# Kernel tuning notes

Measured on AMD Instinct MI355X. Metric: run time of the kernel, lower is better.

Reference implementation:

```python
import jax, jax.numpy as jnp
import numpy as np

NEG_INF = -1e30
EPS = 1e-5


def _layernorm(x, g, b):
    m = jnp.mean(x, axis=-1, keepdims=True)
    v = jnp.var(x, axis=-1, keepdims=True)
    return (x - m) * jax.lax.rsqrt(v + EPS) * g + b


def _mlp(x, w1, b1, w2, b2):
    h = jax.nn.gelu(x @ w1.T + b1, approximate=False)
    return h @ w2.T + b2


def _sparse_attn(q, k, v, scale, window):
    # q: [N,H,Q,hd], k/v: [N,H,K,hd]
    scores = jnp.einsum('nhqd,nhkd->nhqk', q, k) * scale
    scores = jnp.clip(scores, -10000.0, 10000.0)
    Q, K = scores.shape[-2], scores.shape[-1]
    i = jnp.arange(Q)[:, None]
    j = jnp.arange(K)[None, :]
    # row i < K: sliding window of radius `window`; row i >= K: fully unmasked
    allowed = (i >= K) | ((j >= i - window) & (j <= i + window))
    scores = jnp.where(allowed, scores, NEG_INF)
    w = jax.nn.softmax(scores, axis=-1)
    w = jnp.nan_to_num(w, nan=0.0, posinf=10000.0, neginf=-10000.0)
    out = jnp.einsum('nhqk,nhkd->nhqd', w, v)
    return jnp.nan_to_num(out, nan=0.0, posinf=10000.0, neginf=-10000.0)


B, T, L, D = 8, 96, 128, 256
H = 2
HD = D // H
FACTOR = 10
WINDOW = 5
DFF = 4 * D


def setup_inputs() -> dict:
    key = jax.random.key(0)
    ks = jax.random.split(key, 16)
    s = 0.02
    inp = {
        'x': jax.random.normal(ks[0], (B, T, L, D), jnp.float32),
        'router': jax.random.normal(ks[1], (L, FACTOR, D), jnp.float32),
        'Wr': jax.random.normal(ks[2], (D, D), jnp.float32) * s,
        'br': jnp.zeros((D,), jnp.float32),
        'Wk': jax.random.normal(ks[3], (D, D), jnp.float32) * s,
        'bk': jnp.zeros((D,), jnp.float32),
        'Wv': jax.random.normal(ks[4], (D, D), jnp.float32) * s,
        'bv': jnp.zeros((D,), jnp.float32),
        'Wq': jax.random.normal(ks[5], (D, D), jnp.float32) * s,
        'bq': jnp.zeros((D,), jnp.float32),
        'g1': jnp.ones((D,), jnp.float32), 'beta1': jnp.zeros((D,), jnp.float32),
        'g2': jnp.ones((D,), jnp.float32), 'beta2': jnp.zeros((D,), jnp.float32),
        'g3': jnp.ones((D,), jnp.float32), 'beta3': jnp.zeros((D,), jnp.float32),
        'm1_w1': jax.random.normal(ks[6], (DFF, D), jnp.float32) * s,
        'm1_b1': jnp.zeros((DFF,), jnp.float32),
        'm1_w2': jax.random.normal(ks[7], (D, DFF), jnp.float32) * s,
        'm1_b2': jnp.zeros((D,), jnp.float32),
        'm2_w1': jax.random.normal(ks[8], (DFF, D), jnp.float32) * s,
        'm2_b1': jnp.zeros((DFF,), jnp.float32),
        'm2_w2': jax.random.normal(ks[9], (D, DFF), jnp.float32) * s,
        'm2_b2': jnp.zeros((D,), jnp.float32),
    }
    return inp


def reference(x, router, Wr, br, Wk, bk, Wv, bv, Wq, bq,
              g1, beta1, g2, beta2, g3, beta3,
              m1_w1, m1_b1, m1_w2, m1_b2,
              m2_w1, m2_b1, m2_w2, m2_b2):
    b, t, l, d = x.shape
    scale = HD ** (-0.5)
    # b t l d -> (b l) t d
    x_dim = jnp.transpose(x, (0, 2, 1, 3)).reshape(b * l, t, d)
    x_proj = _layernorm(x_dim + _mlp(x_dim, m1_w1, m1_b1, m1_w2, m1_b2), g1, beta1)
    keys = (x_proj @ Wk.T + bk).reshape(b * l, t, H, HD).transpose(0, 2, 1, 3)
    values = (x_proj @ Wv.T + bv).reshape(b * l, t, H, HD).transpose(0, 2, 1, 3)
    router_b = jnp.broadcast_to(router, (b, l, FACTOR, d)).reshape(b * l, FACTOR, d)
    router_proj = (router_b @ Wr.T + br).reshape(b * l, FACTOR, H, HD).transpose(0, 2, 1, 3)
    sender = _sparse_attn(router_proj, keys, values, scale, WINDOW)  # [BL,H,F,HD]
    query = (x_proj @ Wq.T + bq).reshape(b * l, t, H, HD).transpose(0, 2, 1, 3)
    recv = _sparse_attn(query, sender, sender, scale, WINDOW)  # [BL,H,T,HD]
    recv = recv.transpose(0, 2, 1, 3).reshape(b * l, t, d)
    x_upd = _layernorm(x_proj + _mlp(recv, m2_w1, m2_b1, m2_w2, m2_b2), g2, beta2)
    out = x_upd.reshape(b, l, t, d).transpose(0, 2, 1, 3)
    return _layernorm(out, g3, beta3)
```

## Files before the change

### kernel.cpp

```cpp
#include <hip/hip_runtime.h>
#include <math.h>

#define B_ 8
#define T_ 96
#define L_ 128
#define D_ 256
#define H_ 2
#define HD_ 128
#define F_ 10
#define DFF_ 1024
#define BL_ 1024
#define M_ 98304
#define SCALE_ 0.08838834764831845f

typedef __attribute__((ext_vector_type(4))) float f32x4;
typedef __attribute__((ext_vector_type(8))) short bf16x8;
typedef __attribute__((ext_vector_type(4))) unsigned short u16x4;

__device__ __forceinline__ unsigned short f2bf(float f) {
  union { float f; unsigned int u; } v; v.f = f;
  unsigned int r = v.u + 0x7fffu + ((v.u >> 16) & 1u);
  return (unsigned short)(r >> 16);
}
__device__ __forceinline__ float bf2f(unsigned short s) {
  union { unsigned int u; float f; } v; v.u = ((unsigned int)s) << 16;
  return v.f;
}
__device__ __forceinline__ f32x4 mfma16(bf16x8 a, bf16x8 b, f32x4 c) {
  return __builtin_amdgcn_mfma_f32_16x16x32_bf16(a, b, c, 0, 0, 0);
}
__device__ __forceinline__ float wave_sum(float v) {
  #pragma unroll
  for (int m = 1; m < 64; m <<= 1) v += __shfl_xor(v, m, 64);
  return v;
}

__global__ void f2bf_kernel(const float* __restrict__ src,
                            unsigned short* __restrict__ dst, int n) {
  int i = blockIdx.x * 256 + threadIdx.x;
  if (i < n) dst[i] = f2bf(src[i]);
}

template<int MODE>
__launch_bounds__(256, 2)
__global__ void mlp_ln_kernel(
    const float* __restrict__ xin,
    const unsigned short* __restrict__ ain_bf,
    const unsigned short* __restrict__ res_bf,
    const unsigned short* __restrict__ w1,
    const float* __restrict__ b1,
    const unsigned short* __restrict__ w2,
    const float* __restrict__ b2,
    const float* __restrict__ gA, const float* __restrict__ bA,
    const float* __restrict__ gB, const float* __restrict__ bB,
    unsigned short* __restrict__ out_bf,
    float* __restrict__ out_f32)
{
  __shared__ __align__(16) unsigned char smem[65536];
  unsigned short* As = (unsigned short*)smem;
  unsigned short* Hs = (unsigned short*)(smem + 32768);
  float* Ys = (float*)smem;

  const int tid = threadIdx.x;
  const int m0 = blockIdx.x * 64;

  #pragma unroll
  for (int it = 0; it < 8; ++it) {
    int u = tid + it * 256;
    int row = u >> 5, k = (u & 31) * 8;
    bf16x8 v;
    if constexpr (MODE == 1) {
      int m = m0 + row;
      int bb_ = m / (L_ * T_);
      int rem = m - bb_ * (L_ * T_);
      int li = rem / T_;
      int tt = rem - li * T_;
      const float* p = xin + (((size_t)((bb_ * T_ + tt) * L_ + li)) << 8) + k;
      #pragma unroll
      for (int i = 0; i < 8; ++i) v[i] = (short)f2bf(p[i]);
    } else {
      v = *(const bf16x8*)(ain_bf + (size_t)(m0 + row) * D_ + k);
    }
    *(bf16x8*)(As + ((row * D_ + k) ^ ((row & 7) << 3))) = v;
  }
  __syncthreads();

  const int wid = tid >> 6;
  const int lane = tid & 63;
  const int lr = lane & 15;
  const int lk = lane >> 4;

  f32x4 acc_y[4][4];
  #pragma unroll
  for (int nf = 0; nf < 4; ++nf) {
    float bb = b2[wid * 64 + nf * 16 + lr];
    #pragma unroll
    for (int mf = 0; mf < 4; ++mf) acc_y[mf][nf] = (f32x4){bb, bb, bb, bb};
  }

  #pragma unroll 1
  for (int c = 0; c < 4; ++c) {
    f32x4 acc_h[4][4];
    #pragma unroll
    for (int nf = 0; nf < 4; ++nf) {
      float bb = b1[c * 256 + wid * 64 + nf * 16 + lr];
      #pragma unroll
      for (int mf = 0; mf < 4; ++mf) acc_h[mf][nf] = (f32x4){bb, bb, bb, bb};
    }
    #pragma unroll
    for (int ks = 0; ks < 8; ++ks) {
      bf16x8 a[4], bfr[4];
      #pragma unroll
      for (int mf = 0; mf < 4; ++mf) {
        int row = mf * 16 + lr;
        a[mf] = *(const bf16x8*)(As + ((row * D_ + ks * 32 + lk * 8) ^ ((row & 7) << 3)));
      }
      #pragma unroll
      for (int nf = 0; nf < 4; ++nf) {
        int n1 = c * 256 + wid * 64 + nf * 16 + lr;
        bfr[nf] = *(const bf16x8*)(w1 + (size_t)n1 * D_ + ks * 32 + lk * 8);
      }
      #pragma unroll
      for (int mf = 0; mf < 4; ++mf)
        #pragma unroll
        for (int nf = 0; nf < 4; ++nf)
          acc_h[mf][nf] = mfma16(a[mf], bfr[nf], acc_h[mf][nf]);
    }
    #pragma unroll
    for (int mf = 0; mf < 4; ++mf)
      #pragma unroll
      for (int nf = 0; nf < 4; ++nf)
        #pragma unroll
        for (int j = 0; j < 4; ++j) {
          int row = mf * 16 + lk * 4 + j;
          int col = wid * 64 + nf * 16 + lr;
          float v = acc_h[mf][nf][j];
          float g = 0.5f * v * (1.0f + erff(v * 0.70710678118654752f));
          Hs[(row * D_ + col) ^ ((row & 7) << 3)] = f2bf(g);
        }
    __syncthreads();
    #pragma unroll
    for (int ks = 0; ks < 8; ++ks) {
      bf16x8 a[4], bfr[4];
      #pragma unroll
      for (int mf = 0; mf < 4; ++mf) {
        int row = mf * 16 + lr;
        a[mf] = *(const bf16x8*)(Hs + ((row * D_ + ks * 32 + lk * 8) ^ ((row & 7) << 3)));
      }
      #pragma unroll
      for (int nf = 0; nf < 4; ++nf) {
        int n2 = wid * 64 + nf * 16 + lr;
        bfr[nf] = *(const bf16x8*)(w2 + (size_t)n2 * DFF_ + c * 256 + ks * 32 + lk * 8);
      }
      #pragma unroll
      for (int mf = 0; mf < 4; ++mf)
        #pragma unroll
        for (int nf = 0; nf < 4; ++nf)
          acc_y[mf][nf] = mfma16(a[mf], bfr[nf], acc_y[mf][nf]);
    }
    __syncthreads();
  }

  #pragma unroll
  for (int mf = 0; mf < 4; ++mf)
    #pragma unroll
    for (int nf = 0; nf < 4; ++nf)
      #pragma unroll
      for (int j = 0; j < 4; ++j) {
        int row = mf * 16 + lk * 4 + j;
        int col = wid * 64 + nf * 16 + lr;
        Ys[row * 256 + col] = acc_y[mf][nf][j];
      }
  __syncthreads();

  const float4 gAv = *(const float4*)(gA + lane * 4);
  const float4 bAv = *(const float4*)(bA + lane * 4);
  float4 gBv = {0.f, 0.f, 0.f, 0.f}, bBv = {0.f, 0.f, 0.f, 0.f};
  if constexpr (MODE == 2) {
    gBv = *(const float4*)(gB + lane * 4);
    bBv = *(const float4*)(bB + lane * 4);
  }

  #pragma unroll 1
  for (int i = 0; i < 16; ++i) {
    int row = wid * 16 + i;
    int m = m0 + row;
    int bb_ = m / (L_ * T_);
    int rem = m - bb_ * (L_ * T_);
    int li = rem / T_;
    int tt = rem - li * T_;
    size_t xoff = ((size_t)((bb_ * T_ + tt) * L_ + li)) << 8;
    const float* yr = Ys + row * 256 + lane * 4;
    float v0 = yr[0], v1 = yr[1], v2 = yr[2], v3 = yr[3];
    if constexpr (MODE == 1) {
      float4 r = *(const float4*)(xin + xoff + lane * 4);
      v0 += r.x; v1 += r.y; v2 += r.z; v3 += r.w;
    } else {
      u16x4 r = *(const u16x4*)(res_bf + (size_t)m * D_ + lane * 4);
      v0 += bf2f(r[0]); v1 += bf2f(r[1]); v2 += bf2f(r[2]); v3 += bf2f(r[3]);
    }
    float s = v0 + v1 + v2 + v3;
    float q = v0 * v0 + v1 * v1 + v2 * v2 + v3 * v3;
    s = wave_sum(s); q = wave_sum(q);
    float mean = s * (1.0f / 256.0f);
    float var = q * (1.0f / 256.0f) - mean * mean;
    float rstd = rsqrtf(var + 1e-5f);
    float u0 = (v0 - mean) * rstd * gAv.x + bAv.x;
    float u1 = (v1 - mean) * rstd * gAv.y + bAv.y;
    float u2 = (v2 - mean) * rstd * gAv.z + bAv.z;
    float u3 = (v3 - mean) * rstd * gAv.w + bAv.w;
    if constexpr (MODE == 1) {
      u16x4 o;
      o[0] = f2bf(u0); o[1] = f2bf(u1); o[2] = f2bf(u2); o[3] = f2bf(u3);
      *(u16x4*)(out_bf + (size_t)m * D_ + lane * 4) = o;
    } else {
      float s2 = u0 + u1 + u2 + u3;
      float q2 = u0 * u0 + u1 * u1 + u2 * u2 + u3 * u3;
      s2 = wave_sum(s2); q2 = wave_sum(q2);
      float mean2 = s2 * (1.0f / 256.0f);
      float var2 = q2 * (1.0f / 256.0f) - mean2 * mean2;
      float rstd2 = rsqrtf(var2 + 1e-5f);
      float4 o;
      o.x = (u0 - mean2) * rstd2 * gBv.x + bBv.x;
      o.y = (u1 - mean2) * rstd2 * gBv.y + bBv.y;
      o.z = (u2 - mean2) * rstd2 * gBv.z + bBv.z;
      o.w = (u3 - mean2) * rstd2 * gBv.w + bBv.w;
      *(float4*)(out_f32 + xoff + lane * 4) = o;
    }
  }
}

template<int WHICH>
__launch_bounds__(256, 2)
__global__ void proj_kernel(const unsigned short* __restrict__ ain,
                            const float* __restrict__ ain_f,
                            const unsigned short* __restrict__ wbf,
                            const float* __restrict__ bias,
                            unsigned short* __restrict__ outp)
{
  __shared__ __align__(16) unsigned short As[64 * 256];
  const int tid = threadIdx.x;
  const int m0 = blockIdx.x * 64;
  #pragma unroll
  for (int it = 0; it < 8; ++it) {
    int u = tid + it * 256;
    int row = u >> 5, k = (u & 31) * 8;
    bf16x8 v;
    if constexpr (WHICH == 3) {
      const float* p = ain_f + (size_t)(m0 + row) * D_ + k;
      #pragma unroll
      for (int i = 0; i < 8; ++i) v[i] = (short)f2bf(p[i]);
    } else {
      v = *(const bf16x8*)(ain + (size_t)(m0 + row) * D_ + k);
    }
    *(bf16x8*)(As + ((row * D_ + k) ^ ((row & 7) << 3))) = v;
  }
  __syncthreads();
  const int wid = tid >> 6, lane = tid & 63, lr = lane & 15, lk = lane >> 4;
  f32x4 acc[4][4];
  #pragma unroll
  for (int nf = 0; nf < 4; ++nf) {
    float bb = bias[wid * 64 + nf * 16 + lr];
    #pragma unroll
    for (int mf = 0; mf < 4; ++mf) acc[mf][nf] = (f32x4){bb, bb, bb, bb};
  }
  #pragma unroll
  for (int ks = 0; ks < 8; ++ks) {
    bf16x8 a[4], bfr[4];
    #pragma unroll
    for (int mf = 0; mf < 4; ++mf) {
      int row = mf * 16 + lr;
      a[mf] = *(const bf16x8*)(As + ((row * D_ + ks * 32 + lk * 8) ^ ((row & 7) << 3)));
    }
    #pragma unroll
    for (int nf = 0; nf < 4; ++nf) {
      int n = wid * 64 + nf * 16 + lr;
      bfr[nf] = *(const bf16x8*)(wbf + (size_t)n * D_ + ks * 32 + lk * 8);
    }
    #pragma unroll
    for (int mf = 0; mf < 4; ++mf)
      #pragma unroll
      for (int nf = 0; nf < 4; ++nf)
        acc[mf][nf] = mfma16(a[mf], bfr[nf], acc[mf][nf]);
  }
  #pragma unroll
  for (int mf = 0; mf < 4; ++mf)
    #pragma unroll
    for (int nf = 0; nf < 4; ++nf)
      #pragma unroll
      for (int j = 0; j < 4; ++j) {
        int m = m0 + mf * 16 + lk * 4 + j;
        int n = wid * 64 + nf * 16 + lr;
        unsigned short val = f2bf(acc[mf][nf][j]);
        int h = n >> 7, hd = n & 127;
        if constexpr (WHICH < 3) {
          int bl = m / T_, t = m - bl * T_;
          outp[(size_t)((bl * 2 + h) * T_ + t) * HD_ + hd] = val;
        } else {
          int li = m / F_, f = m - li * F_;
          outp[(size_t)((li * 2 + h) * F_ + f) * HD_ + hd] = val;
        }
      }
}

__global__ void sender_kernel(const unsigned short* __restrict__ Kb,
                              const unsigned short* __restrict__ Vb,
                              const unsigned short* __restrict__ Rp,
                              unsigned short* __restrict__ Sd)
{
  __shared__ float Ks[15 * 128];
  __shared__ float Vs[15 * 128];
  const int bh = blockIdx.x;
  const int l = (bh >> 1) & (L_ - 1);
  const int h = bh & 1;
  const int tid = threadIdx.x;
  for (int u = tid; u < 15 * 128; u += 256) {
    Ks[u] = bf2f(Kb[(size_t)bh * T_ * HD_ + u]);
    Vs[u] = bf2f(Vb[(size_t)bh * T_ * HD_ + u]);
  }
  __syncthreads();
  const int wid = tid >> 6, lane = tid & 63;
  const int d0 = lane * 2;
  for (int f = wid; f < F_; f += 4) {
    float q0 = bf2f(Rp[(size_t)((l * 2 + h) * F_ + f) * HD_ + d0]);
    float q1 = bf2f(Rp[(size_t)((l * 2 + h) * F_ + f) * HD_ + d0 + 1]);
    float sc[11];
    #pragma unroll
    for (int jj = 0; jj < 11; ++jj) {
      int j = f - 5 + jj;
      int jc = j < 0 ? 0 : j;
      float p = q0 * Ks[jc * 128 + d0] + q1 * Ks[jc * 128 + d0 + 1];
      float r = wave_sum(p) * SCALE_;
      r = fminf(fmaxf(r, -10000.0f), 10000.0f);
      sc[jj] = (j >= 0) ? r : -1e30f;
    }
    float mx = sc[0];
    #pragma unroll
    for (int jj = 1; jj < 11; ++jj) mx = fmaxf(mx, sc[jj]);
    float pr[11], se = 0.0f;
    #pragma unroll
    for (int jj = 0; jj < 11; ++jj) { pr[jj] = __expf(sc[jj] - mx); se += pr[jj]; }
    float inv = 1.0f / se;
    float o0 = 0.0f, o1 = 0.0f;
    #pragma unroll
    for (int jj = 0; jj < 11; ++jj) {
      int j = f - 5 + jj;
      int jc = j < 0 ? 0 : j;
      float w = pr[jj] * inv;
      o0 += w * Vs[jc * 128 + d0];
      o1 += w * Vs[jc * 128 + d0 + 1];
    }
    unsigned int pk = (unsigned int)f2bf(o0) | ((unsigned int)f2bf(o1) << 16);
    *(unsigned int*)(Sd + (size_t)(bh * F_ + f) * HD_ + d0) = pk;
  }
}

__global__ void recv_kernel(const unsigned short* __restrict__ Qb,
                            const unsigned short* __restrict__ Sd,
                            unsigned short* __restrict__ Rv)
{
  __shared__ float Ss[F_ * 128];
  const int bh = blockIdx.x;
  const int bl = bh >> 1, h = bh & 1;
  const int tid = threadIdx.x;
  for (int u = tid; u < F_ * 128; u += 256) Ss[u] = bf2f(Sd[(size_t)bh * F_ * HD_ + u]);
  __syncthreads();
  const int wid = tid >> 6, lane = tid & 63;
  const int d0 = lane * 2;
  for (int t = wid; t < T_; t += 4) {
    float q0 = bf2f(Qb[(size_t)(bh * T_ + t) * HD_ + d0]);
    float q1 = bf2f(Qb[(size_t)(bh * T_ + t) * HD_ + d0 + 1]);
    float sc[10];
    #pragma unroll
    for (int j = 0; j < 10; ++j) {
      float p = q0 * Ss[j * 128 + d0] + q1 * Ss[j * 128 + d0 + 1];
      float r = wave_sum(p) * SCALE_;
      r = fminf(fmaxf(r, -10000.0f), 10000.0f);
      bool allowed = (t >= 10) || ((j >= t - 5) && (j <= t + 5));
      sc[j] = allowed ? r : -1e30f;
    }
    float mx = sc[0];
    #pragma unroll
    for (int j = 1; j < 10; ++j) mx = fmaxf(mx, sc[j]);
    float pr[10], se = 0.0f;
    #pragma unroll
    for (int j = 0; j < 10; ++j) { pr[j] = __expf(sc[j] - mx); se += pr[j]; }
    float inv = 1.0f / se;
    float o0 = 0.0f, o1 = 0.0f;
    #pragma unroll
    for (int j = 0; j < 10; ++j) {
      float w = pr[j] * inv;
      o0 += w * Ss[j * 128 + d0];
      o1 += w * Ss[j * 128 + d0 + 1];
    }
    unsigned int pk = (unsigned int)f2bf(o0) | ((unsigned int)f2bf(o1) << 16);
    *(unsigned int*)(Rv + (size_t)(bl * T_ + t) * D_ + h * HD_ + d0) = pk;
  }
}

extern "C" void kernel_launch(void* const* d_in, const int* in_sizes, int n_in,
                              void* d_out, int out_size, void* d_ws, size_t ws_size,
                              hipStream_t stream) {
  const float* x      = (const float*)d_in[0];
  const float* router = (const float*)d_in[1];
  const float* Wr     = (const float*)d_in[2];
  const float* br     = (const float*)d_in[3];
  const float* Wk     = (const float*)d_in[4];
  const float* bk     = (const float*)d_in[5];
  const float* Wv     = (const float*)d_in[6];
  const float* bv     = (const float*)d_in[7];
  const float* Wq     = (const float*)d_in[8];
  const float* bq     = (const float*)d_in[9];
  const float* g1     = (const float*)d_in[10];
  const float* beta1  = (const float*)d_in[11];
  const float* g2     = (const float*)d_in[12];
  const float* beta2  = (const float*)d_in[13];
  const float* g3     = (const float*)d_in[14];
  const float* beta3  = (const float*)d_in[15];
  const float* m1_w1  = (const float*)d_in[16];
  const float* m1_b1  = (const float*)d_in[17];
  const float* m1_w2  = (const float*)d_in[18];
  const float* m1_b2  = (const float*)d_in[19];
  const float* m2_w1  = (const float*)d_in[20];
  const float* m2_b1  = (const float*)d_in[21];
  const float* m2_w2  = (const float*)d_in[22];
  const float* m2_b2  = (const float*)d_in[23];
  float* out = (float*)d_out;

  char* ws = (char*)d_ws;
  unsigned short* w1a   = (unsigned short*)(ws + 0);
  unsigned short* w1b   = (unsigned short*)(ws + 524288);
  unsigned short* w2a   = (unsigned short*)(ws + 1048576);
  unsigned short* w2b   = (unsigned short*)(ws + 1572864);
  unsigned short* wkb   = (unsigned short*)(ws + 2097152);
  unsigned short* wvb   = (unsigned short*)(ws + 2228224);
  unsigned short* wqb   = (unsigned short*)(ws + 2359296);
  unsigned short* wrb   = (unsigned short*)(ws + 2490368);
  unsigned short* xproj = (unsigned short*)(ws + 2621440);
  unsigned short* kbuf  = (unsigned short*)(ws + 52953088);
  unsigned short* vbuf  = (unsigned short*)(ws + 103284736);
  unsigned short* qbuf  = (unsigned short*)(ws + 153616384);
  unsigned short* sdbuf = (unsigned short*)(ws + 203948032);
  unsigned short* rpbuf = (unsigned short*)(ws + 209190912);

  f2bf_kernel<<<1024, 256, 0, stream>>>(m1_w1, w1a, 262144);
  f2bf_kernel<<<1024, 256, 0, stream>>>(m1_w2, w1b, 262144);
  f2bf_kernel<<<1024, 256, 0, stream>>>(m2_w1, w2a, 262144);
  f2bf_kernel<<<1024, 256, 0, stream>>>(m2_w2, w2b, 262144);
  f2bf_kernel<<<256, 256, 0, stream>>>(Wk, wkb, 65536);
  f2bf_kernel<<<256, 256, 0, stream>>>(Wv, wvb, 65536);
  f2bf_kernel<<<256, 256, 0, stream>>>(Wq, wqb, 65536);
  f2bf_kernel<<<256, 256, 0, stream>>>(Wr, wrb, 65536);

  mlp_ln_kernel<1><<<M_ / 64, 256, 0, stream>>>(
      x, nullptr, nullptr, w1a, m1_b1, w1b, m1_b2,
      g1, beta1, nullptr, nullptr, xproj, nullptr);

  proj_kernel<0><<<M_ / 64, 256, 0, stream>>>(xproj, nullptr, wkb, bk, kbuf);
  proj_kernel<1><<<M_ / 64, 256, 0, stream>>>(xproj, nullptr, wvb, bv, vbuf);
  proj_kernel<2><<<M_ / 64, 256, 0, stream>>>(xproj, nullptr, wqb, bq, qbuf);
  proj_kernel<3><<<(L_ * F_) / 64, 256, 0, stream>>>(nullptr, router, wrb, br, rpbuf);

  sender_kernel<<<BL_ * H_, 256, 0, stream>>>(kbuf, vbuf, rpbuf, sdbuf);

  unsigned short* recv = kbuf;
  recv_kernel<<<BL_ * H_, 256, 0, stream>>>(qbuf, sdbuf, recv);

  mlp_ln_kernel<2><<<M_ / 64, 256, 0, stream>>>(
      nullptr, recv, xproj, w2a, m2_b1, w2b, m2_b2,
      g2, beta2, g3, beta3, nullptr, out);
}
```

Baseline: 954.4 us.

## Fuse QKV projections and attention stages, shrink MLP smem, store only needed K/V rows

Merges the eight weight-conversion launches into one kernel and the three Q/K/V projections into a single kernel that reuses the shared-memory activation tile. K and V are written only for the first 15 time steps, the only ones the windowed sender attention reads. The sender and receiver attention kernels are fused so sender outputs stay in shared memory. The MLP kernel uses a 128-wide hidden chunk with smaller shared memory to allow three blocks per CU, replaces erff with a polynomial erf approximation, and keeps the MLP output plus residual in bf16 in shared memory instead of fp32. The bf16 rounding of that pre-layernorm sum and the approximate erf add some numerical error.

```diff
diff --git a/kernel.cpp b/kernel.cpp
--- a/kernel.cpp
+++ b/kernel.cpp
@@ -11,6 +11,7 @@
 #define DFF_ 1024
 #define BL_ 1024
 #define M_ 98304
+#define KV_ 15
 #define SCALE_ 0.08838834764831845f
 
 typedef __attribute__((ext_vector_type(4))) float f32x4;
@@ -34,15 +35,39 @@
   for (int m = 1; m < 64; m <<= 1) v += __shfl_xor(v, m, 64);
   return v;
 }
-
-__global__ void f2bf_kernel(const float* __restrict__ src,
-                            unsigned short* __restrict__ dst, int n) {
+__device__ __forceinline__ float gelu_f(float v) {
+  float x = v * 0.70710678118654752f;
+  float ax = fabsf(x);
+  float t = __builtin_amdgcn_rcpf(1.0f + 0.3275911f * ax);
+  float y = t * (0.254829592f + t * (-0.284496736f + t * (1.421413741f +
+            t * (-1.453152027f + t * 1.061405429f))));
+  float er = 1.0f - y * __expf(-x * x);
+  er = copysignf(er, x);
+  return 0.5f * v * (1.0f + er);
+}
+
+__global__ void f2bf_all_kernel(const float* __restrict__ s0, const float* __restrict__ s1,
+                                const float* __restrict__ s2, const float* __restrict__ s3,
+                                const float* __restrict__ s4, const float* __restrict__ s5,
+                                const float* __restrict__ s6, const float* __restrict__ s7,
+                                unsigned short* __restrict__ dst) {
   int i = blockIdx.x * 256 + threadIdx.x;
-  if (i < n) dst[i] = f2bf(src[i]);
+  const float* src; int base;
+  if (i < 1048576) {
+    int seg = i >> 18;
+    src = seg == 0 ? s0 : seg == 1 ? s1 : seg == 2 ? s2 : s3;
+    base = seg << 18;
+  } else {
+    int j = i - 1048576;
+    int seg = j >> 16;
+    src = seg == 0 ? s4 : seg == 1 ? s5 : seg == 2 ? s6 : s7;
+    base = 1048576 + (seg << 16);
+  }
+  dst[i] = f2bf(src[i - base]);
 }
 
 template<int MODE>
-__launch_bounds__(256, 2)
+__launch_bounds__(256, 3)
 __global__ void mlp_ln_kernel(
     const float* __restrict__ xin,
     const unsigned short* __restrict__ ain_bf,
@@ -56,10 +81,8 @@
     unsigned short* __restrict__ out_bf,
     float* __restrict__ out_f32)
 {
-  __shared__ __align__(16) unsigned char smem[65536];
-  unsigned short* As = (unsigned short*)smem;
-  unsigned short* Hs = (unsigned short*)(smem + 32768);
-  float* Ys = (float*)smem;
+  __shared__ __align__(16) unsigned short As[64 * 256];
+  __shared__ __align__(16) unsigned short Hs[64 * 128];
 
   const int tid = threadIdx.x;
   const int m0 = blockIdx.x * 64;
@@ -99,58 +122,56 @@
   }
 
   #pragma unroll 1
-  for (int c = 0; c < 4; ++c) {
-    f32x4 acc_h[4][4];
-    #pragma unroll
-    for (int nf = 0; nf < 4; ++nf) {
-      float bb = b1[c * 256 + wid * 64 + nf * 16 + lr];
+  for (int c = 0; c < 8; ++c) {
+    f32x4 acc_h[4][2];
+    #pragma unroll
+    for (int nf = 0; nf < 2; ++nf) {
+      float bb = b1[c * 128 + wid * 32 + nf * 16 + lr];
       #pragma unroll
       for (int mf = 0; mf < 4; ++mf) acc_h[mf][nf] = (f32x4){bb, bb, bb, bb};
     }
     #pragma unroll
     for (int ks = 0; ks < 8; ++ks) {
-      bf16x8 a[4], bfr[4];
+      bf16x8 a[4], bfr[2];
       #pragma unroll
       for (int mf = 0; mf < 4; ++mf) {
         int row = mf * 16 + lr;
         a[mf] = *(const bf16x8*)(As + ((row * D_ + ks * 32 + lk * 8) ^ ((row & 7) << 3)));
       }
       #pragma unroll
-      for (int nf = 0; nf < 4; ++nf) {
-        int n1 = c * 256 + wid * 64 + nf * 16 + lr;
+      for (int nf = 0; nf < 2; ++nf) {
+        int n1 = c * 128 + wid * 32 + nf * 16 + lr;
         bfr[nf] = *(const bf16x8*)(w1 + (size_t)n1 * D_ + ks * 32 + lk * 8);
       }
       #pragma unroll
       for (int mf = 0; mf < 4; ++mf)
         #pragma unroll
-        for (int nf = 0; nf < 4; ++nf)
+        for (int nf = 0; nf < 2; ++nf)
           acc_h[mf][nf] = mfma16(a[mf], bfr[nf], acc_h[mf][nf]);
     }
     #pragma unroll
     for (int mf = 0; mf < 4; ++mf)
       #pragma unroll
-      for (int nf = 0; nf < 4; ++nf)
+      for (int nf = 0; nf < 2; ++nf)
         #pragma unroll
         for (int j = 0; j < 4; ++j) {
           int row = mf * 16 + lk * 4 + j;
-          int col = wid * 64 + nf * 16 + lr;
-          float v = acc_h[mf][nf][j];
-          float g = 0.5f * v * (1.0f + erff(v * 0.70710678118654752f));
-          Hs[(row * D_ + col) ^ ((row & 7) << 3)] = f2bf(g);
+          int col = wid * 32 + nf * 16 + lr;
+          Hs[(row * 128 + col) ^ ((row & 7) << 3)] = f2bf(gelu_f(acc_h[mf][nf][j]));
         }
     __syncthreads();
     #pragma unroll
-    for (int ks = 0; ks < 8; ++ks) {
+    for (int ks = 0; ks < 4; ++ks) {
       bf16x8 a[4], bfr[4];
       #pragma unroll
       for (int mf = 0; mf < 4; ++mf) {
         int row = mf * 16 + lr;
-        a[mf] = *(const bf16x8*)(Hs + ((row * D_ + ks * 32 + lk * 8) ^ ((row & 7) << 3)));
+        a[mf] = *(const bf16x8*)(Hs + ((row * 128 + ks * 32 + lk * 8) ^ ((row & 7) << 3)));
       }
       #pragma unroll
       for (int nf = 0; nf < 4; ++nf) {
         int n2 = wid * 64 + nf * 16 + lr;
-        bfr[nf] = *(const bf16x8*)(w2 + (size_t)n2 * DFF_ + c * 256 + ks * 32 + lk * 8);
+        bfr[nf] = *(const bf16x8*)(w2 + (size_t)n2 * DFF_ + c * 128 + ks * 32 + lk * 8);
       }
       #pragma unroll
       for (int mf = 0; mf < 4; ++mf)
@@ -169,7 +190,10 @@
       for (int j = 0; j < 4; ++j) {
         int row = mf * 16 + lk * 4 + j;
         int col = wid * 64 + nf * 16 + lr;
-        Ys[row * 256 + col] = acc_y[mf][nf][j];
+        int idx = (row * D_ + col) ^ ((row & 7) << 3);
+        float v = acc_y[mf][nf][j];
+        if constexpr (MODE == 1) v += bf2f(As[idx]);
+        As[idx] = f2bf(v);
       }
   __syncthreads();
 
@@ -185,17 +209,10 @@
   for (int i = 0; i < 16; ++i) {
     int row = wid * 16 + i;
     int m = m0 + row;
-    int bb_ = m / (L_ * T_);
-    int rem = m - bb_ * (L_ * T_);
-    int li = rem / T_;
-    int tt = rem - li * T_;
-    size_t xoff = ((size_t)((bb_ * T_ + tt) * L_ + li)) << 8;
-    const float* yr = Ys + row * 256 + lane * 4;
-    float v0 = yr[0], v1 = yr[1], v2 = yr[2], v3 = yr[3];
-    if constexpr (MODE == 1) {
-      float4 r = *(const float4*)(xin + xoff + lane * 4);
-      v0 += r.x; v1 += r.y; v2 += r.z; v3 += r.w;
-    } else {
+    int idx = (row * D_ + lane * 4) ^ ((row & 7) << 3);
+    u16x4 yv = *(const u16x4*)(As + idx);
+    float v0 = bf2f(yv[0]), v1 = bf2f(yv[1]), v2 = bf2f(yv[2]), v3 = bf2f(yv[3]);
+    if constexpr (MODE == 2) {
       u16x4 r = *(const u16x4*)(res_bf + (size_t)m * D_ + lane * 4);
       v0 += bf2f(r[0]); v1 += bf2f(r[1]); v2 += bf2f(r[2]); v3 += bf2f(r[3]);
     }
@@ -220,6 +237,11 @@
       float mean2 = s2 * (1.0f / 256.0f);
       float var2 = q2 * (1.0f / 256.0f) - mean2 * mean2;
       float rstd2 = rsqrtf(var2 + 1e-5f);
+      int bb_ = m / (L_ * T_);
+      int rem = m - bb_ * (L_ * T_);
+      int li = rem / T_;
+      int tt = rem - li * T_;
+      size_t xoff = ((size_t)((bb_ * T_ + tt) * L_ + li)) << 8;
       float4 o;
       o.x = (u0 - mean2) * rstd2 * gBv.x + bBv.x;
       o.y = (u1 - mean2) * rstd2 * gBv.y + bBv.y;
@@ -230,13 +252,65 @@
   }
 }
 
-template<int WHICH>
-__launch_bounds__(256, 2)
-__global__ void proj_kernel(const unsigned short* __restrict__ ain,
-                            const float* __restrict__ ain_f,
-                            const unsigned short* __restrict__ wbf,
-                            const float* __restrict__ bias,
-                            unsigned short* __restrict__ outp)
+__device__ __forceinline__ void proj_one(
+    const unsigned short* As, const unsigned short* __restrict__ w,
+    const float* __restrict__ bias, unsigned short* __restrict__ outp,
+    bool kv15, int m0, int wid, int lane)
+{
+  const int lr = lane & 15, lk = lane >> 4;
+  f32x4 acc[4][4];
+  #pragma unroll
+  for (int nf = 0; nf < 4; ++nf) {
+    float bb = bias[wid * 64 + nf * 16 + lr];
+    #pragma unroll
+    for (int mf = 0; mf < 4; ++mf) acc[mf][nf] = (f32x4){bb, bb, bb, bb};
+  }
+  #pragma unroll
+  for (int ks = 0; ks < 8; ++ks) {
+    bf16x8 a[4], bfr[4];
+    #pragma unroll
+    for (int mf = 0; mf < 4; ++mf) {
+      int row = mf * 16 + lr;
+      a[mf] = *(const bf16x8*)(As + ((row * D_ + ks * 32 + lk * 8) ^ ((row & 7) << 3)));
+    }
+    #pragma unroll
+    for (int nf = 0; nf < 4; ++nf) {
+      int n = wid * 64 + nf * 16 + lr;
+      bfr[nf] = *(const bf16x8*)(w + (size_t)n * D_ + ks * 32 + lk * 8);
+    }
+    #pragma unroll
+    for (int mf = 0; mf < 4; ++mf)
+      #pragma unroll
+      for (int nf = 0; nf < 4; ++nf)
+        acc[mf][nf] = mfma16(a[mf], bfr[nf], acc[mf][nf]);
+  }
+  #pragma unroll
+  for (int mf = 0; mf < 4; ++mf)
+    #pragma unroll
+    for (int nf = 0; nf < 4; ++nf)
+      #pragma unroll
+      for (int j = 0; j < 4; ++j) {
+        int m = m0 + mf * 16 + lk * 4 + j;
+        int n = wid * 64 + nf * 16 + lr;
+        int h = n >> 7, hd = n & 127;
+        int bl = m / T_, t = m - bl * T_;
+        unsigned short val = f2bf(acc[mf][nf][j]);
+        if (kv15) {
+          if (t < KV_) outp[(size_t)((bl * 2 + h) * KV_ + t) * HD_ + hd] = val;
+        } else {
+          outp[(size_t)((bl * 2 + h) * T_ + t) * HD_ + hd] = val;
+        }
+      }
+}
+
+__launch_bounds__(256, 4)
+__global__ void qkv_kernel(const unsigned short* __restrict__ xproj,
+                           const unsigned short* __restrict__ wk, const float* __restrict__ bk,
+                           unsigned short* __restrict__ ok,
+                           const unsigned short* __restrict__ wv, const float* __restrict__ bv,
+                           unsigned short* __restrict__ ov,
+                           const unsigned short* __restrict__ wq, const float* __restrict__ bq,
+                           unsigned short* __restrict__ oq)
 {
   __shared__ __align__(16) unsigned short As[64 * 256];
   const int tid = threadIdx.x;
@@ -245,14 +319,33 @@
   for (int it = 0; it < 8; ++it) {
     int u = tid + it * 256;
     int row = u >> 5, k = (u & 31) * 8;
+    bf16x8 v = *(const bf16x8*)(xproj + (size_t)(m0 + row) * D_ + k);
+    *(bf16x8*)(As + ((row * D_ + k) ^ ((row & 7) << 3))) = v;
+  }
+  __syncthreads();
+  const int wid = tid >> 6, lane = tid & 63;
+  proj_one(As, wk, bk, ok, true, m0, wid, lane);
+  proj_one(As, wv, bv, ov, true, m0, wid, lane);
+  proj_one(As, wq, bq, oq, false, m0, wid, lane);
+}
+
+__launch_bounds__(256, 4)
+__global__ void router_proj_kernel(const float* __restrict__ router,
+                                   const unsigned short* __restrict__ wbf,
+                                   const float* __restrict__ bias,
+                                   unsigned short* __restrict__ outp)
+{
+  __shared__ __align__(16) unsigned short As[64 * 256];
+  const int tid = threadIdx.x;
+  const int m0 = blockIdx.x * 64;
+  #pragma unroll
+  for (int it = 0; it < 8; ++it) {
+    int u = tid + it * 256;
+    int row = u >> 5, k = (u & 31) * 8;
+    const float* p = router + (size_t)(m0 + row) * D_ + k;
     bf16x8 v;
-    if constexpr (WHICH == 3) {
-      const float* p = ain_f + (size_t)(m0 + row) * D_ + k;
-      #pragma unroll
-      for (int i = 0; i < 8; ++i) v[i] = (short)f2bf(p[i]);
-    } else {
-      v = *(const bf16x8*)(ain + (size_t)(m0 + row) * D_ + k);
-    }
+    #pragma unroll
+    for (int i = 0; i < 8; ++i) v[i] = (short)f2bf(p[i]);
     *(bf16x8*)(As + ((row * D_ + k) ^ ((row & 7) << 3))) = v;
   }
   __syncthreads();
@@ -291,32 +384,29 @@
       for (int j = 0; j < 4; ++j) {
         int m = m0 + mf * 16 + lk * 4 + j;
         int n = wid * 64 + nf * 16 + lr;
-        unsigned short val = f2bf(acc[mf][nf][j]);
         int h = n >> 7, hd = n & 127;
-        if constexpr (WHICH < 3) {
-          int bl = m / T_, t = m - bl * T_;
-          outp[(size_t)((bl * 2 + h) * T_ + t) * HD_ + hd] = val;
-        } else {
-          int li = m / F_, f = m - li * F_;
-          outp[(size_t)((li * 2 + h) * F_ + f) * HD_ + hd] = val;
-        }
-      }
-}
-
-__global__ void sender_kernel(const unsigned short* __restrict__ Kb,
-                              const unsigned short* __restrict__ Vb,
-                              const unsigned short* __restrict__ Rp,
-                              unsigned short* __restrict__ Sd)
+        int li = m / F_, f = m - li * F_;
+        outp[(size_t)((li * 2 + h) * F_ + f) * HD_ + hd] = f2bf(acc[mf][nf][j]);
+      }
+}
+
+__global__ void attn_kernel(const unsigned short* __restrict__ Kb,
+                            const unsigned short* __restrict__ Vb,
+                            const unsigned short* __restrict__ Rp,
+                            const unsigned short* __restrict__ Qb,
+                            unsigned short* __restrict__ Rv)
 {
-  __shared__ float Ks[15 * 128];
-  __shared__ float Vs[15 * 128];
+  __shared__ float Ks[KV_ * 128];
+  __shared__ float Vs[KV_ * 128];
+  __shared__ float Ss[F_ * 128];
   const int bh = blockIdx.x;
-  const int l = (bh >> 1) & (L_ - 1);
+  const int bl = bh >> 1;
+  const int l = bl & (L_ - 1);
   const int h = bh & 1;
   const int tid = threadIdx.x;
-  for (int u = tid; u < 15 * 128; u += 256) {
-    Ks[u] = bf2f(Kb[(size_t)bh * T_ * HD_ + u]);
-    Vs[u] = bf2f(Vb[(size_t)bh * T_ * HD_ + u]);
+  for (int u = tid; u < KV_ * 128; u += 256) {
+    Ks[u] = bf2f(Kb[(size_t)bh * KV_ * HD_ + u]);
+    Vs[u] = bf2f(Vb[(size_t)bh * KV_ * HD_ + u]);
   }
   __syncthreads();
   const int wid = tid >> 6, lane = tid & 63;
@@ -350,23 +440,10 @@
       o0 += w * Vs[jc * 128 + d0];
       o1 += w * Vs[jc * 128 + d0 + 1];
     }
-    unsigned int pk = (unsigned int)f2bf(o0) | ((unsigned int)f2bf(o1) << 16);
-    *(unsigned int*)(Sd + (size_t)(bh * F_ + f) * HD_ + d0) = pk;
-  }
-}
-
-__global__ void recv_kernel(const unsigned short* __restrict__ Qb,
-                            const unsigned short* __restrict__ Sd,
-                            unsigned short* __restrict__ Rv)
-{
-  __shared__ float Ss[F_ * 128];
-  const int bh = blockIdx.x;
-  const int bl = bh >> 1, h = bh & 1;
-  const int tid = threadIdx.x;
-  for (int u = tid; u < F_ * 128; u += 256) Ss[u] = bf2f(Sd[(size_t)bh * F_ * HD_ + u]);
+    Ss[f * 128 + d0] = o0;
+    Ss[f * 128 + d0 + 1] = o1;
+  }
   __syncthreads();
-  const int wid = tid >> 6, lane = tid & 63;
-  const int d0 = lane * 2;
   for (int t = wid; t < T_; t += 4) {
     float q0 = bf2f(Qb[(size_t)(bh * T_ + t) * HD_ + d0]);
     float q1 = bf2f(Qb[(size_t)(bh * T_ + t) * HD_ + d0 + 1]);
@@ -428,6 +505,7 @@
   float* out = (float*)d_out;
 
   char* ws = (char*)d_ws;
+  unsigned short* wbase = (unsigned short*)ws;
   unsigned short* w1a   = (unsigned short*)(ws + 0);
   unsigned short* w1b   = (unsigned short*)(ws + 524288);
   unsigned short* w2a   = (unsigned short*)(ws + 1048576);
@@ -438,35 +516,25 @@
   unsigned short* wrb   = (unsigned short*)(ws + 2490368);
   unsigned short* xproj = (unsigned short*)(ws + 2621440);
   unsigned short* kbuf  = (unsigned short*)(ws + 52953088);
-  unsigned short* vbuf  = (unsigned short*)(ws + 103284736);
-  unsigned short* qbuf  = (unsigned short*)(ws + 153616384);
-  unsigned short* sdbuf = (unsigned short*)(ws + 203948032);
-  unsigned short* rpbuf = (unsigned short*)(ws + 209190912);
-
-  f2bf_kernel<<<1024, 256, 0, stream>>>(m1_w1, w1a, 262144);
-  f2bf_kernel<<<1024, 256, 0, stream>>>(m1_w2, w1b, 262144);
-  f2bf_kernel<<<1024, 256, 0, stream>>>(m2_w1, w2a, 262144);
-  f2bf_kernel<<<1024, 256, 0, stream>>>(m2_w2, w2b, 262144);
-  f2bf_kernel<<<256, 256, 0, stream>>>(Wk, wkb, 65536);
-  f2bf_kernel<<<256, 256, 0, stream>>>(Wv, wvb, 65536);
-  f2bf_kernel<<<256, 256, 0, stream>>>(Wq, wqb, 65536);
-  f2bf_kernel<<<256, 256, 0, stream>>>(Wr, wrb, 65536);
+  unsigned short* vbuf  = (unsigned short*)(ws + 60817408);
+  unsigned short* qbuf  = (unsigned short*)(ws + 68681728);
+  unsigned short* rvbuf = (unsigned short*)(ws + 119013376);
+  unsigned short* rpbuf = (unsigned short*)(ws + 169345024);
+
+  f2bf_all_kernel<<<5120, 256, 0, stream>>>(m1_w1, m1_w2, m2_w1, m2_w2,
+                                            Wk, Wv, Wq, Wr, wbase);
 
   mlp_ln_kernel<1><<<M_ / 64, 256, 0, stream>>>(
       x, nullptr, nullptr, w1a, m1_b1, w1b, m1_b2,
       g1, beta1, nullptr, nullptr, xproj, nullptr);
 
-  proj_kernel<0><<<M_ / 64, 256, 0, stream>>>(xproj, nullptr, wkb, bk, kbuf);
-  proj_kernel<1><<<M_ / 64, 256, 0, stream>>>(xproj, nullptr, wvb, bv, vbuf);
-  proj_kernel<2><<<M_ / 64, 256, 0, stream>>>(xproj, nullptr, wqb, bq, qbuf);
-  proj_kernel<3><<<(L_ * F_) / 64, 256, 0, stream>>>(nullptr, router, wrb, br, rpbuf);
-
-  sender_kernel<<<BL_ * H_, 256, 0, stream>>>(kbuf, vbuf, rpbuf, sdbuf);
-
-  unsigned short* recv = kbuf;
-  recv_kernel<<<BL_ * H_, 256, 0, stream>>>(qbuf, sdbuf, recv);
+  qkv_kernel<<<M_ / 64, 256, 0, stream>>>(xproj, wkb, bk, kbuf, wvb, bv, vbuf,
+                                          wqb, bq, qbuf);
+  router_proj_kernel<<<(L_ * F_) / 64, 256, 0, stream>>>(router, wrb, br, rpbuf);
+
+  attn_kernel<<<BL_ * H_, 256, 0, stream>>>(kbuf, vbuf, rpbuf, qbuf, rvbuf);
 
   mlp_ln_kernel<2><<<M_ / 64, 256, 0, stream>>>(
-      nullptr, recv, xproj, w2a, m2_b1, w2b, m2_b2,
+      nullptr, rvbuf, xproj, w2a, m2_b1, w2b, m2_b2,
       g2, beta2, g3, beta3, nullptr, out);
 }
```

Result: slower. 1.349 ms (+41.3%).
